# Optimization experiments

Hardware: AMD Instinct MI355X
Metric: run time of the kernel (lower is better)

## Reference

```python
import jax, jax.numpy as jnp
import numpy as np

N, E = 100000, 1000000          # nodes, edges
IN, OUT = 64, 64                # feature dims
R, B = 16, 8                    # num_rels, num_bases


def setup_inputs() -> dict:
    key = jax.random.key(0)
    k = jax.random.split(key, 6)
    h = jax.random.normal(k[0], (N, IN), jnp.float32)
    weight = jax.random.normal(k[1], (B, IN, OUT), jnp.float32) * 0.05
    w_comp = jax.random.normal(k[2], (R, B), jnp.float32) * 0.3
    src = jax.random.randint(k[3], (E,), 0, N, jnp.int32)
    dst = jax.random.randint(k[4], (E,), 0, N, jnp.int32)
    rel = jax.random.randint(k[5], (E,), 0, R, jnp.int32)
    return {"h": h, "weight": weight, "w_comp": w_comp,
            "src": src, "dst": dst, "rel": rel}


def _rel_weights(weight, w_comp):
    # Faithful replication of the torch basis-combination including its
    # exact (reinterpreting) view calls:
    #   weight.view(in, B, out); matmul(w_comp, .); .view(R, in, out)
    V = weight.reshape(IN, B, OUT)                 # reinterpret, not transpose
    M = jnp.einsum('rb,ibo->iro', w_comp, V)       # [IN, R, OUT]
    return M.reshape(R, IN, OUT)


def reference(h, weight, w_comp, src, dst, rel):
    W = _rel_weights(weight, w_comp)               # [R, IN, OUT]
    # msg_e = h[src_e] @ W[rel_e]; computed without materializing [E,IN,OUT]:
    proj = jnp.einsum('nd,rdf->nrf', h, W)         # [N, R, OUT]
    msg = proj[src, rel]                           # [E, OUT] per-edge gather
    h2 = jax.ops.segment_sum(msg, dst, num_segments=N)  # fn.sum -> 'h2'
    # apply_func: bias is None (falsy); returns activation(old h).
    # Note: original apply_func reads but does not use h2 (tutorial quirk);
    # we return both the updated 'h' and the aggregated 'h2'.
    h_new = jax.nn.relu(h)
    return h_new, h2
```

## Files before the change

kernel.cpp:

```cpp
#include <hip/hip_runtime.h>
#include <hip/hip_bf16.h>

#define NN 100000
#define EE 1000000
#define FDIM 64
#define NREL 16
#define NBASE 8
#define HN (NN * FDIM)
#define H4 (HN / 4)
#define WSZ (NREL * FDIM * FDIM)
#define GX 96

__global__ void zero_counts_kernel(int* counts) {
    if (threadIdx.x < NREL) counts[threadIdx.x] = 0;
}

__global__ void compute_w_kernel(const float* __restrict__ weight,
                                 const float* __restrict__ w_comp,
                                 float* __restrict__ W) {
    int q = blockIdx.x * blockDim.x + threadIdx.x;
    if (q >= WSZ) return;
    int i = q >> 10;
    int r = (q >> 6) & 15;
    int o = q & 63;
    float acc = 0.f;
#pragma unroll
    for (int b = 0; b < NBASE; ++b)
        acc = fmaf(w_comp[r * NBASE + b], weight[i * 512 + b * 64 + o], acc);
    W[q] = acc;
}

__global__ void relu_zero_kernel(const float4* __restrict__ h4,
                                 float4* __restrict__ out4) {
    int i = blockIdx.x * blockDim.x + threadIdx.x;
    if (i < H4) {
        float4 v = h4[i];
        v.x = fmaxf(v.x, 0.f); v.y = fmaxf(v.y, 0.f);
        v.z = fmaxf(v.z, 0.f); v.w = fmaxf(v.w, 0.f);
        out4[i] = v;
        out4[H4 + i] = make_float4(0.f, 0.f, 0.f, 0.f);
    }
}

__global__ void hist_kernel(const int* __restrict__ rel, int* __restrict__ counts) {
    __shared__ int lc[NREL];
    if (threadIdx.x < NREL) lc[threadIdx.x] = 0;
    __syncthreads();
    int stride = gridDim.x * blockDim.x;
    for (int i = blockIdx.x * blockDim.x + threadIdx.x; i < EE; i += stride)
        atomicAdd(&lc[rel[i]], 1);
    __syncthreads();
    if (threadIdx.x < NREL && lc[threadIdx.x] > 0)
        atomicAdd(&counts[threadIdx.x], lc[threadIdx.x]);
}

__global__ void scan_kernel(const int* __restrict__ counts,
                            int* __restrict__ offsets, int* __restrict__ cursors) {
    if (threadIdx.x == 0 && blockIdx.x == 0) {
        int acc = 0;
        for (int r = 0; r < NREL; ++r) { offsets[r] = acc; cursors[r] = acc; acc += counts[r]; }
        offsets[NREL] = acc;
    }
}

__global__ void scatter_kernel(const int* __restrict__ rel, const int* __restrict__ src,
                               const int* __restrict__ dst, int* __restrict__ cursors,
                               int* __restrict__ src_bin, int* __restrict__ dst_bin) {
    __shared__ int lhist[NREL];
    __shared__ int lbase[NREL];
    int i = blockIdx.x * blockDim.x + threadIdx.x;
    if (threadIdx.x < NREL) lhist[threadIdx.x] = 0;
    __syncthreads();
    int r = 0, rank = 0;
    if (i < EE) { r = rel[i]; rank = atomicAdd(&lhist[r], 1); }
    __syncthreads();
    if (threadIdx.x < NREL && lhist[threadIdx.x] > 0)
        lbase[threadIdx.x] = atomicAdd(&cursors[threadIdx.x], lhist[threadIdx.x]);
    __syncthreads();
    if (i < EE) {
        int pos = lbase[r] + rank;
        src_bin[pos] = src[i];
        dst_bin[pos] = dst[i];
    }
}

__global__ __launch_bounds__(256) void edge_kernel(
    const int* __restrict__ offsets, const int* __restrict__ src_bin,
    const int* __restrict__ dst_bin, const float* __restrict__ h,
    const float* __restrict__ W, float* __restrict__ h2) {
    const int rel = blockIdx.y;
    const int lane = threadIdx.x & 63;
    const int start = offsets[rel];
    const int end = offsets[rel + 1];

    float wcol[FDIM];
    const float* wbase = W + rel * 4096 + lane;
#pragma unroll
    for (int d = 0; d < FDIM; ++d) wcol[d] = wbase[d * 64];

    const int nw = GX * 4;
    const int wave = blockIdx.x * 4 + (threadIdx.x >> 6);
    const int cnt = end - start;
    const int per = (cnt + nw - 1) / nw;
    int i0 = start + wave * per;
    int i1 = i0 + per; if (i1 > end) i1 = end;

    for (int i = i0; i < i1; ++i) {
        int s  = __builtin_amdgcn_readfirstlane(src_bin[i]);
        int dv = __builtin_amdgcn_readfirstlane(dst_bin[i]);
        const float* __restrict__ hrow = h + (size_t)s * FDIM;
        float a0 = 0.f, a1 = 0.f, a2 = 0.f, a3 = 0.f;
#pragma unroll
        for (int d = 0; d < FDIM; d += 4) {
            a0 = fmaf(hrow[d],     wcol[d],     a0);
            a1 = fmaf(hrow[d + 1], wcol[d + 1], a1);
            a2 = fmaf(hrow[d + 2], wcol[d + 2], a2);
            a3 = fmaf(hrow[d + 3], wcol[d + 3], a3);
        }
        float acc = (a0 + a1) + (a2 + a3);
        unsafeAtomicAdd(&h2[(size_t)dv * FDIM + lane], acc);
    }
}

extern "C" void kernel_launch(void* const* d_in, const int* in_sizes, int n_in,
                              void* d_out, int out_size, void* d_ws, size_t ws_size,
                              hipStream_t stream) {
    const float* h      = (const float*)d_in[0];
    const float* weight = (const float*)d_in[1];
    const float* w_comp = (const float*)d_in[2];
    const int*   src    = (const int*)d_in[3];
    const int*   dst    = (const int*)d_in[4];
    const int*   rel    = (const int*)d_in[5];

    float* out_hnew = (float*)d_out;
    float* out_h2   = out_hnew + HN;

    float* W       = (float*)d_ws;
    int*   meta    = (int*)((char*)d_ws + WSZ * 4);
    int*   counts  = meta;
    int*   offsets = meta + 16;
    int*   cursors = meta + 33;
    int*   src_bin = (int*)((char*)d_ws + WSZ * 4 + 256);
    int*   dst_bin = src_bin + EE;

    hipLaunchKernelGGL(zero_counts_kernel, dim3(1), dim3(64), 0, stream, counts);
    hipLaunchKernelGGL(compute_w_kernel, dim3(WSZ / 256), dim3(256), 0, stream,
                       weight, w_comp, W);
    hipLaunchKernelGGL(relu_zero_kernel, dim3((H4 + 255) / 256), dim3(256), 0, stream,
                       (const float4*)h, (float4*)out_hnew);
    hipLaunchKernelGGL(hist_kernel, dim3(1024), dim3(256), 0, stream, rel, counts);
    hipLaunchKernelGGL(scan_kernel, dim3(1), dim3(64), 0, stream, counts, offsets, cursors);
    hipLaunchKernelGGL(scatter_kernel, dim3((EE + 255) / 256), dim3(256), 0, stream,
                       rel, src, dst, cursors, src_bin, dst_bin);
    hipLaunchKernelGGL(edge_kernel, dim3(GX, NREL), dim3(256), 0, stream,
                       offsets, src_bin, dst_bin, h, W, out_h2);
}
```

Before: 392.3 us.

## Use bf16 MFMA for per-edge projection over 16-edge tiles

Rewrites the edge kernel so each wave handles 16 edges of one relation at a time, running bf16 16x16x32 MFMAs against a transposed bf16 per-relation weight held in registers. The old path did one scalar 64-wide dot product per edge. Node features are converted to bf16 inside the relu pass, which halves gather bandwidth. The counts-zeroing launch is folded into the weight kernel and the grid grows. Rounding both operands to bf16 adds precision error, and writing the bf16 copy of h costs extra memory traffic.

Result: faster. 374.6 us (-4.5%).

```diff
diff --git a/kernel.cpp b/kernel.cpp
--- a/kernel.cpp
+++ b/kernel.cpp
@@ -9,32 +9,45 @@
 #define HN (NN * FDIM)
 #define H4 (HN / 4)
 #define WSZ (NREL * FDIM * FDIM)
-#define GX 96
+#define EGX 128
 
-__global__ void zero_counts_kernel(int* counts) {
-    if (threadIdx.x < NREL) counts[threadIdx.x] = 0;
+typedef __attribute__((ext_vector_type(8))) short short8;
+typedef __attribute__((ext_vector_type(4))) float f32x4;
+
+static __device__ __forceinline__ ushort f2bf(float f) {
+    __hip_bfloat16 b = __float2bfloat16(f);
+    return *(ushort*)&b;
 }
 
-__global__ void compute_w_kernel(const float* __restrict__ weight,
-                                 const float* __restrict__ w_comp,
-                                 float* __restrict__ W) {
+__global__ void compute_wt_kernel(const float* __restrict__ weight,
+                                  const float* __restrict__ w_comp,
+                                  ushort* __restrict__ WT, int* __restrict__ counts) {
     int q = blockIdx.x * blockDim.x + threadIdx.x;
+    if (blockIdx.x == 0 && threadIdx.x < NREL) counts[threadIdx.x] = 0;
     if (q >= WSZ) return;
-    int i = q >> 10;
-    int r = (q >> 6) & 15;
-    int o = q & 63;
+    int r = q >> 12;
+    int o = (q >> 6) & 63;
+    int d = q & 63;
+    const float* wc = w_comp + (d & 15) * NBASE;
+    const float* wv = weight + (size_t)(4 * r + (d >> 4)) * 512 + o;
     float acc = 0.f;
 #pragma unroll
     for (int b = 0; b < NBASE; ++b)
-        acc = fmaf(w_comp[r * NBASE + b], weight[i * 512 + b * 64 + o], acc);
-    W[q] = acc;
+        acc = fmaf(wc[b], wv[b * 64], acc);
+    WT[q] = f2bf(acc);
 }
 
-__global__ void relu_zero_kernel(const float4* __restrict__ h4,
-                                 float4* __restrict__ out4) {
+__global__ void relu_zero_cvt_kernel(const float4* __restrict__ h4,
+                                     float4* __restrict__ out4,
+                                     ushort2* __restrict__ hb2) {
     int i = blockIdx.x * blockDim.x + threadIdx.x;
     if (i < H4) {
         float4 v = h4[i];
+        ushort2 lo, hi;
+        lo.x = f2bf(v.x); lo.y = f2bf(v.y);
+        hi.x = f2bf(v.z); hi.y = f2bf(v.w);
+        hb2[2 * i] = lo;
+        hb2[2 * i + 1] = hi;
         v.x = fmaxf(v.x, 0.f); v.y = fmaxf(v.y, 0.f);
         v.z = fmaxf(v.z, 0.f); v.w = fmaxf(v.w, 0.f);
         out4[i] = v;
@@ -84,41 +97,66 @@
     }
 }
 
-__global__ __launch_bounds__(256) void edge_kernel(
+__global__ __launch_bounds__(256) void edge_mfma_kernel(
     const int* __restrict__ offsets, const int* __restrict__ src_bin,
-    const int* __restrict__ dst_bin, const float* __restrict__ h,
-    const float* __restrict__ W, float* __restrict__ h2) {
-    const int rel = blockIdx.y;
+    const int* __restrict__ dst_bin, const ushort* __restrict__ hb,
+    const ushort* __restrict__ WT, float* __restrict__ h2) {
+    const int rel  = blockIdx.y;
     const int lane = threadIdx.x & 63;
+    const int quad = lane >> 4;
+    const int l15  = lane & 15;
     const int start = offsets[rel];
-    const int end = offsets[rel + 1];
+    const int end   = offsets[rel + 1];
+    const int cnt   = end - start;
+    if (cnt <= 0) return;
 
-    float wcol[FDIM];
-    const float* wbase = W + rel * 4096 + lane;
+    const short8* wt = (const short8*)(WT + rel * 4096);
+    short8 Bf[2][4];
 #pragma unroll
-    for (int d = 0; d < FDIM; ++d) wcol[d] = wbase[d * 64];
+    for (int t = 0; t < 4; ++t) {
+#pragma unroll
+        for (int s = 0; s < 2; ++s)
+            Bf[s][t] = wt[((t * 16 + l15) << 3) + (s << 2) + quad];
+    }
 
-    const int nw = GX * 4;
+    const int nw   = EGX * 4;
     const int wave = blockIdx.x * 4 + (threadIdx.x >> 6);
-    const int cnt = end - start;
-    const int per = (cnt + nw - 1) / nw;
-    int i0 = start + wave * per;
-    int i1 = i0 + per; if (i1 > end) i1 = end;
+    const int nb   = (cnt + 15) >> 4;
+    const int per  = (nb + nw - 1) / nw;
+    int b0 = wave * per;
+    int b1 = b0 + per; if (b1 > nb) b1 = nb;
 
-    for (int i = i0; i < i1; ++i) {
-        int s  = __builtin_amdgcn_readfirstlane(src_bin[i]);
-        int dv = __builtin_amdgcn_readfirstlane(dst_bin[i]);
-        const float* __restrict__ hrow = h + (size_t)s * FDIM;
-        float a0 = 0.f, a1 = 0.f, a2 = 0.f, a3 = 0.f;
+    const int quad4 = quad * 4;
+
+    for (int b = b0; b < b1; ++b) {
+        const int base = start + (b << 4);
+        int ei = base + l15; if (ei >= end) ei = end - 1;
+        int s0 = src_bin[ei];
+        const short8* ar = (const short8*)(hb + (size_t)s0 * FDIM);
+        short8 A0 = ar[quad];
+        short8 A1 = ar[4 + quad];
+
+        f32x4 acc[4];
 #pragma unroll
-        for (int d = 0; d < FDIM; d += 4) {
-            a0 = fmaf(hrow[d],     wcol[d],     a0);
-            a1 = fmaf(hrow[d + 1], wcol[d + 1], a1);
-            a2 = fmaf(hrow[d + 2], wcol[d + 2], a2);
-            a3 = fmaf(hrow[d + 3], wcol[d + 3], a3);
+        for (int t = 0; t < 4; ++t) acc[t] = (f32x4){0.f, 0.f, 0.f, 0.f};
+#pragma unroll
+        for (int t = 0; t < 4; ++t) {
+            acc[t] = __builtin_amdgcn_mfma_f32_16x16x32_bf16(A0, Bf[0][t], acc[t], 0, 0, 0);
+            acc[t] = __builtin_amdgcn_mfma_f32_16x16x32_bf16(A1, Bf[1][t], acc[t], 0, 0, 0);
         }
-        float acc = (a0 + a1) + (a2 + a3);
-        unsafeAtomicAdd(&h2[(size_t)dv * FDIM + lane], acc);
+
+#pragma unroll
+        for (int r = 0; r < 4; ++r) {
+            int em = base + quad4 + r;
+            if (em < end) {
+                int dv = dst_bin[em];
+                float* p = h2 + (size_t)dv * FDIM + l15;
+                unsafeAtomicAdd(p,      acc[0][r]);
+                unsafeAtomicAdd(p + 16, acc[1][r]);
+                unsafeAtomicAdd(p + 32, acc[2][r]);
+                unsafeAtomicAdd(p + 48, acc[3][r]);
+            }
+        }
     }
 }
 
@@ -135,23 +173,24 @@
     float* out_hnew = (float*)d_out;
     float* out_h2   = out_hnew + HN;
 
-    float* W       = (float*)d_ws;
-    int*   meta    = (int*)((char*)d_ws + WSZ * 4);
-    int*   counts  = meta;
-    int*   offsets = meta + 16;
-    int*   cursors = meta + 33;
-    int*   src_bin = (int*)((char*)d_ws + WSZ * 4 + 256);
-    int*   dst_bin = src_bin + EE;
+    char* ws = (char*)d_ws;
+    ushort* WT      = (ushort*)ws;
+    int*    meta    = (int*)(ws + 0x20000);
+    int*    counts  = meta;
+    int*    offsets = meta + 16;
+    int*    cursors = meta + 33;
+    int*    src_bin = (int*)(ws + 0x20400);
+    int*    dst_bin = (int*)(ws + 0x20400 + 4 * EE);
+    ushort* hb      = (ushort*)(ws + 0x20400 + 8 * EE);
 
-    hipLaunchKernelGGL(zero_counts_kernel, dim3(1), dim3(64), 0, stream, counts);
-    hipLaunchKernelGGL(compute_w_kernel, dim3(WSZ / 256), dim3(256), 0, stream,
-                       weight, w_comp, W);
-    hipLaunchKernelGGL(relu_zero_kernel, dim3((H4 + 255) / 256), dim3(256), 0, stream,
-                       (const float4*)h, (float4*)out_hnew);
+    hipLaunchKernelGGL(compute_wt_kernel, dim3(WSZ / 256), dim3(256), 0, stream,
+                       weight, w_comp, WT, counts);
+    hipLaunchKernelGGL(relu_zero_cvt_kernel, dim3((H4 + 255) / 256), dim3(256), 0, stream,
+                       (const float4*)h, (float4*)out_hnew, (ushort2*)hb);
     hipLaunchKernelGGL(hist_kernel, dim3(1024), dim3(256), 0, stream, rel, counts);
     hipLaunchKernelGGL(scan_kernel, dim3(1), dim3(64), 0, stream, counts, offsets, cursors);
     hipLaunchKernelGGL(scatter_kernel, dim3((EE + 255) / 256), dim3(256), 0, stream,
                        rel, src, dst, cursors, src_bin, dst_bin);
-    hipLaunchKernelGGL(edge_kernel, dim3(GX, NREL), dim3(256), 0, stream,
-                       offsets, src_bin, dst_bin, h, W, out_h2);
+    hipLaunchKernelGGL(edge_mfma_kernel, dim3(EGX, NREL), dim3(256), 0, stream,
+                       offsets, src_bin, dst_bin, hb, WT, out_h2);
 }
```
